# Performance work log

Hardware: AMD Instinct MI355X
Metric: run time of the kernel (lower is better)

Reference implementation:

```python
import jax, jax.numpy as jnp
import numpy as np

D_MODEL, D_INNER, D_STATE, HEADDIM, NHEADS, D_CONV, EPS = 2048, 4096, 64, 64, 64, 4, 1e-5
CONV_DIM = D_INNER + 2 * D_STATE  # ngroups=1


def setup_inputs() -> dict:
    key = jax.random.key(0)
    ks = jax.random.split(key, 8)
    return {
        "hidden_states": jax.random.normal(ks[0], (2, 2048, D_MODEL), jnp.float32),
        "rms_weight": jnp.ones((D_MODEL,), jnp.float32),
        "in_proj_w": jax.random.normal(ks[1], (2 * D_INNER + 2 * D_STATE + NHEADS, D_MODEL), jnp.float32) * 0.02,
        "conv_w": jax.random.normal(ks[2], (CONV_DIM, D_CONV), jnp.float32) * 0.2,
        "conv_b": jnp.zeros((CONV_DIM,), jnp.float32),
        "dt_bias": jax.random.normal(ks[3], (NHEADS,), jnp.float32) * 0.5,
        "A_log": jax.random.uniform(ks[4], (NHEADS,), jnp.float32, 0.0, 1.0),
        "D": jnp.ones((NHEADS,), jnp.float32),
        "norm_w": jnp.ones((D_INNER,), jnp.float32),
        "out_proj_w": jax.random.normal(ks[5], (D_MODEL, D_INNER), jnp.float32) * 0.02,
    }


def _rmsnorm(x, w, eps=EPS):
    var = jnp.mean(jnp.square(x), axis=-1, keepdims=True)
    return x * jax.lax.rsqrt(var + eps) * w


def reference(hidden_states, rms_weight, in_proj_w, conv_w, conv_b, dt_bias, A_log, D, norm_w, out_proj_w):
    b, l, _ = hidden_states.shape
    residual = hidden_states
    u = _rmsnorm(hidden_states, rms_weight)
    zxbcdt = jnp.einsum("bld,ed->ble", u, in_proj_w)
    z = zxbcdt[..., :D_INNER]
    xBC = zxbcdt[..., D_INNER:D_INNER + CONV_DIM]
    dt = zxbcdt[..., D_INNER + CONV_DIM:]  # (b, l, h)

    # causal depthwise conv1d over seq
    xBC_t = jnp.transpose(xBC, (0, 2, 1))  # (b, c, l)
    kernel = conv_w[:, None, :]  # (c, 1, k)
    xBC_t = jax.lax.conv_general_dilated(
        xBC_t, kernel, window_strides=(1,), padding=[(D_CONV - 1, 0)],
        feature_group_count=CONV_DIM,
        dimension_numbers=("NCH", "OIH", "NCH"))
    xBC = jax.nn.silu(jnp.transpose(xBC_t, (0, 2, 1)) + conv_b)

    x = xBC[..., :D_INNER].reshape(b, l, NHEADS, HEADDIM)
    B = xBC[..., D_INNER:D_INNER + D_STATE]  # (b, l, n)
    C = xBC[..., D_INNER + D_STATE:]         # (b, l, n)

    dt = jax.nn.softplus(dt + dt_bias)  # (b, l, h)
    A = -jnp.exp(A_log)                 # (h,)
    dA = jnp.exp(dt * A)                # (b, l, h)

    # sequential selective scan over time
    def step(state, inp):
        dA_t, dt_t, x_t, B_t, C_t = inp  # (b,h), (b,h), (b,h,p), (b,n), (b,n)
        state = state * dA_t[:, :, None, None] + jnp.einsum(
            "bh,bhp,bn->bhpn", dt_t, x_t, B_t)
        y_t = jnp.einsum("bhpn,bn->bhp", state, C_t)
        return state, y_t

    xs = (jnp.moveaxis(dA, 1, 0), jnp.moveaxis(dt, 1, 0),
          jnp.moveaxis(x, 1, 0), jnp.moveaxis(B, 1, 0), jnp.moveaxis(C, 1, 0))
    state0 = jnp.zeros((b, NHEADS, HEADDIM, D_STATE), hidden_states.dtype)
    _, ys = jax.lax.scan(step, state0, xs)
    y = jnp.moveaxis(ys, 0, 1)  # (b, l, h, p)
    y = y + D[None, None, :, None] * x
    y = y.reshape(b, l, D_INNER)

    # gated RMSNorm, then output projection
    y = _rmsnorm(y * jax.nn.silu(z), norm_w)
    out = jnp.einsum("ble,de->bld", y, out_proj_w)
    return residual + out
```

## Files before the change

kernel.cpp:

```cpp
#include <hip/hip_runtime.h>
#include <stdint.h>

#define DEV static __device__ __forceinline__

typedef __attribute__((ext_vector_type(8))) __bf16 bf16x8;
typedef __attribute__((ext_vector_type(4))) float f32x4;
typedef __attribute__((ext_vector_type(16))) float f32x16;

DEV float b2f(unsigned short u) {
    union { unsigned int i; float f; } v; v.i = ((unsigned int)u) << 16; return v.f;
}
DEV unsigned short f2b(float f) {
    unsigned int u = __builtin_bit_cast(unsigned int, f);
    unsigned int r = (u + 0x7FFFu + ((u >> 16) & 1u)) >> 16;
    return (unsigned short)r;
}
DEV f32x4 mfma16(bf16x8 a, bf16x8 b, f32x4 c) {
    return __builtin_amdgcn_mfma_f32_16x16x32_bf16(a, b, c, 0, 0, 0);
}
DEV f32x16 mfma32(bf16x8 a, bf16x8 b, f32x16 c) {
    return __builtin_amdgcn_mfma_f32_32x32x16_bf16(a, b, c, 0, 0, 0);
}

DEV void gload16(const void* g, void* l) {
    __builtin_amdgcn_global_load_lds(
        (const __attribute__((address_space(1))) void*)g,
        (__attribute__((address_space(3))) void*)l, 16, 0, 0);
}

__global__ __launch_bounds__(256) void k_cvt(
    const float* __restrict__ src, unsigned short* __restrict__ dst)
{
    long i = ((long)blockIdx.x * 256 + threadIdx.x) * 8;
    float4 a = *(const float4*)(src + i);
    float4 b = *(const float4*)(src + i + 4);
    union { uint4 v; unsigned short s[8]; } o;
    o.s[0] = f2b(a.x); o.s[1] = f2b(a.y); o.s[2] = f2b(a.z); o.s[3] = f2b(a.w);
    o.s[4] = f2b(b.x); o.s[5] = f2b(b.y); o.s[6] = f2b(b.z); o.s[7] = f2b(b.w);
    *(uint4*)(dst + i) = o.v;
}

__global__ __launch_bounds__(256) void k_rmsnorm_in(
    const float* __restrict__ h, const float* __restrict__ w,
    unsigned short* __restrict__ u)
{
    int row = blockIdx.x, t = threadIdx.x;
    const float* hp = h + (long)row * 2048 + t * 8;
    float4 a = *(const float4*)hp;
    float4 b = *(const float4*)(hp + 4);
    float x[8] = {a.x, a.y, a.z, a.w, b.x, b.y, b.z, b.w};
    float ss = 0.f;
#pragma unroll
    for (int i = 0; i < 8; i++) ss += x[i] * x[i];
#pragma unroll
    for (int o = 32; o > 0; o >>= 1) ss += __shfl_down(ss, o);
    __shared__ float red[4];
    if ((t & 63) == 0) red[t >> 6] = ss;
    __syncthreads();
    float tot = red[0] + red[1] + red[2] + red[3];
    float scale = rsqrtf(tot * (1.0f / 2048.0f) + 1e-5f);
    float4 wa = *(const float4*)(w + t * 8);
    float4 wb = *(const float4*)(w + t * 8 + 4);
    float wv[8] = {wa.x, wa.y, wa.z, wa.w, wb.x, wb.y, wb.z, wb.w};
    union { uint4 v; unsigned short s[8]; } ow;
#pragma unroll
    for (int i = 0; i < 8; i++) ow.s[i] = f2b(x[i] * scale * wv[i]);
    *(uint4*)(u + (long)row * 2048 + t * 8) = ow.v;
}

template <int EPI>
__global__ __launch_bounds__(256) void k_gemm_bt(
    const unsigned short* __restrict__ A, const unsigned short* __restrict__ Bm,
    int K, int nvalid, unsigned short* __restrict__ Cb, float* __restrict__ Cf,
    int ldc, const float* __restrict__ Res)
{
    __shared__ __align__(16) unsigned short sA[128 * 32];
    __shared__ __align__(16) unsigned short sB[128 * 32];
    int t = threadIdx.x;
    int w = t >> 6, L = t & 63;

    int flat = blockIdx.y * gridDim.x + blockIdx.x;
    int per = gridDim.x * 8;
    int strip = flat / per;
    int rem = flat - strip * per;
    long m0 = (long)(strip * 8 + (rem & 7)) * 128;
    long n0 = (long)(rem >> 3) * 128;

    int rS = w * 32 + (L >> 2);
    int cS = (L & 3) * 8;
    long rB0 = n0 + rS;       if (rB0 >= nvalid) rB0 = nvalid - 1;
    long rB1 = n0 + rS + 16;  if (rB1 >= nvalid) rB1 = nvalid - 1;
    const unsigned short* gA0 = A + (m0 + rS) * K + cS;
    const unsigned short* gA1 = gA0 + 16L * K;
    const unsigned short* gB0 = Bm + rB0 * K + cS;
    const unsigned short* gB1 = Bm + rB1 * K + cS;
    unsigned short* lA0 = sA + (w * 32) * 32 + L * 8;
    unsigned short* lA1 = lA0 + 16 * 32;
    unsigned short* lB0 = sB + (w * 32) * 32 + L * 8;
    unsigned short* lB1 = lB0 + 16 * 32;

    int mw = (w >> 1) * 64, nw = (w & 1) * 64;
    const unsigned short* fA = sA + (mw + (L & 31)) * 32 + (L >> 5) * 8;
    const unsigned short* fB = sB + (nw + (L & 31)) * 32 + (L >> 5) * 8;

    f32x16 acc[2][2];
#pragma unroll
    for (int ti = 0; ti < 2; ti++)
#pragma unroll
        for (int tj = 0; tj < 2; tj++)
#pragma unroll
            for (int r = 0; r < 16; r++) acc[ti][tj][r] = 0.f;

    for (int kt = 0; kt < K; kt += 32) {
        gload16(gA0, lA0); gload16(gA1, lA1);
        gload16(gB0, lB0); gload16(gB1, lB1);
        gA0 += 32; gA1 += 32; gB0 += 32; gB1 += 32;
        __syncthreads();
#pragma unroll
        for (int kk = 0; kk < 2; kk++) {
            bf16x8 af[2], bf[2];
#pragma unroll
            for (int ti = 0; ti < 2; ti++)
                af[ti] = *(const bf16x8*)(fA + ti * 32 * 32 + kk * 16);
#pragma unroll
            for (int tj = 0; tj < 2; tj++)
                bf[tj] = *(const bf16x8*)(fB + tj * 32 * 32 + kk * 16);
#pragma unroll
            for (int ti = 0; ti < 2; ti++)
#pragma unroll
                for (int tj = 0; tj < 2; tj++)
                    acc[ti][tj] = mfma32(af[ti], bf[tj], acc[ti][tj]);
        }
        __syncthreads();
    }
    int colL = L & 31;
    int rL = (L >> 5) * 4;
#pragma unroll
    for (int ti = 0; ti < 2; ti++)
#pragma unroll
        for (int tj = 0; tj < 2; tj++) {
            long c = n0 + nw + tj * 32 + colL;
            if (c >= nvalid) continue;
#pragma unroll
            for (int r = 0; r < 16; r++) {
                long row = m0 + mw + ti * 32 + (r & 3) + 8 * (r >> 2) + rL;
                float v = acc[ti][tj][r];
                if (EPI == 0) Cb[row * ldc + c] = f2b(v);
                else          Cf[row * ldc + c] = v + Res[row * ldc + c];
            }
        }
}

__global__ __launch_bounds__(128) void k_conv(
    const unsigned short* __restrict__ zx, const float* __restrict__ cw,
    const float* __restrict__ cb, unsigned short* __restrict__ xbc)
{
    int c = blockIdx.x * 128 + threadIdx.x;
    int b = blockIdx.z;
    int l0 = blockIdx.y * 64;
    float w0 = cw[c * 4 + 0], w1 = cw[c * 4 + 1];
    float w2 = cw[c * 4 + 2], w3 = cw[c * 4 + 3];
    float bias = cb[c];
    const unsigned short* src = zx + ((long)b * 2048) * 8384 + 4096 + c;
    float xm3 = (l0 >= 3) ? b2f(src[(long)(l0 - 3) * 8384]) : 0.f;
    float xm2 = (l0 >= 2) ? b2f(src[(long)(l0 - 2) * 8384]) : 0.f;
    float xm1 = (l0 >= 1) ? b2f(src[(long)(l0 - 1) * 8384]) : 0.f;
    const unsigned short* s2 = src + (long)l0 * 8384;
    unsigned short* dst = xbc + ((long)(b * 2048 + l0)) * 4224 + c;
#pragma unroll 8
    for (int i = 0; i < 64; i++) {
        float xl = b2f(*s2); s2 += 8384;
        float a = xm3 * w0 + xm2 * w1 + xm1 * w2 + xl * w3 + bias;
        a = a / (1.f + expf(-a));
        *dst = f2b(a); dst += 4224;
        xm3 = xm2; xm2 = xm1; xm1 = xl;
    }
}

__global__ __launch_bounds__(256) void k_chunk_state_mfma(
    const unsigned short* __restrict__ xbc, const unsigned short* __restrict__ zxdt,
    const float* __restrict__ dt_bias, const float* __restrict__ A_log,
    unsigned short* __restrict__ Sbuf, float* __restrict__ dAtot)
{
    int blk = blockIdx.x;
    int c = blk & 7, bh = blk >> 3;
    int b = bh >> 6, h = bh & 63;
    int tid = threadIdx.x;
    int w = tid >> 6, L = tid & 63;
    int quad = L >> 4, col = L & 15;
    int rowBlk = (w >> 1) * 32, colBlk = (w & 1) * 32;
    __shared__ __align__(16) unsigned short sXp[64 * 72];
    __shared__ __align__(16) unsigned short sBn[64 * 72];
    __shared__ float sdt[64], sL[64];
    float Ah = expf(A_log[h]);
    float dtb = dt_bias[h];
    f32x4 acc[2][2];
#pragma unroll
    for (int ti = 0; ti < 2; ti++)
#pragma unroll
        for (int tj = 0; tj < 2; tj++) acc[ti][tj] = (f32x4){0.f, 0.f, 0.f, 0.f};
    float sumL = 0.f;

    for (int sub = 0; sub < 4; sub++) {
        int l0 = c * 256 + sub * 64;
        {
            int t = tid >> 2, pc = tid & 3;
            const unsigned short* gX = xbc + (long)(b * 2048 + l0 + t) * 4224 + h * 64 + pc * 16;
            union { uint4 v; unsigned short s[8]; } x0, x1;
            x0.v = *(const uint4*)gX; x1.v = *(const uint4*)(gX + 8);
#pragma unroll
            for (int j = 0; j < 8; j++) {
                sXp[(pc * 16 + j) * 72 + t] = x0.s[j];
                sXp[(pc * 16 + 8 + j) * 72 + t] = x1.s[j];
            }
        }
        if (tid < 64) {
            float raw = b2f(zxdt[((long)(b * 2048 + l0 + tid)) * 8384 + 8320 + h]) + dtb;
            float dtv = (raw > 20.f) ? raw : log1pf(expf(raw));
            float cum = dtv;
#pragma unroll
            for (int off = 1; off < 64; off <<= 1) {
                float v = __shfl_up(cum, off);
                if (tid >= off) cum += v;
            }
            sdt[tid] = dtv;
            sL[tid] = -Ah * cum;
        }
        __syncthreads();
        float Lend = sL[63];
        {
            int t = tid >> 2, nc = tid & 3;
            float wt = sdt[t] * __expf(Lend - sL[t]);
            const unsigned short* gB = xbc + (long)(b * 2048 + l0 + t) * 4224 + 4096 + nc * 16;
            union { uint4 v; unsigned short s[8]; } x0, x1;
            x0.v = *(const uint4*)gB; x1.v = *(const uint4*)(gB + 8);
#pragma unroll
            for (int j = 0; j < 8; j++) {
                sBn[(nc * 16 + j) * 72 + t] = f2b(b2f(x0.s[j]) * wt);
                sBn[(nc * 16 + 8 + j) * 72 + t] = f2b(b2f(x1.s[j]) * wt);
            }
        }
        __syncthreads();
        float e_end = __expf(Lend);
        sumL += Lend;
#pragma unroll
        for (int ti = 0; ti < 2; ti++)
#pragma unroll
            for (int tj = 0; tj < 2; tj++)
#pragma unroll
                for (int r = 0; r < 4; r++) acc[ti][tj][r] *= e_end;
#pragma unroll
        for (int kb = 0; kb < 2; kb++) {
            bf16x8 ax[2], bx[2];
#pragma unroll
            for (int ti = 0; ti < 2; ti++)
                ax[ti] = *(const bf16x8*)(sXp + (rowBlk + ti * 16 + col) * 72 + kb * 32 + quad * 8);
#pragma unroll
            for (int tj = 0; tj < 2; tj++)
                bx[tj] = *(const bf16x8*)(sBn + (colBlk + tj * 16 + col) * 72 + kb * 32 + quad * 8);
#pragma unroll
            for (int ti = 0; ti < 2; ti++)
#pragma unroll
                for (int tj = 0; tj < 2; tj++)
                    acc[ti][tj] = mfma16(ax[ti], bx[tj], acc[ti][tj]);
        }
        __syncthreads();
    }
#pragma unroll
    for (int ti = 0; ti < 2; ti++)
#pragma unroll
        for (int tj = 0; tj < 2; tj++)
#pragma unroll
            for (int r = 0; r < 4; r++) {
                int p = rowBlk + ti * 16 + quad * 4 + r;
                int n = colBlk + tj * 16 + col;
                Sbuf[(long)blk * 4096 + p * 64 + n] = f2b(acc[ti][tj][r]);
            }
    if (tid == 0) dAtot[blk] = __expf(sumL);
}

__global__ __launch_bounds__(256) void k_scan_chunk_mfma(
    const unsigned short* __restrict__ xbc, const unsigned short* __restrict__ zxdt,
    const float* __restrict__ dt_bias, const float* __restrict__ A_log,
    const float* __restrict__ Dv,
    const unsigned short* __restrict__ Sbuf, const float* __restrict__ dAtot,
    unsigned short* __restrict__ yout)
{
    int blk = blockIdx.x;
    int c = blk & 7, bh = blk >> 3;
    int b = bh >> 6, h = bh & 63;
    int tid = threadIdx.x;
    int w = tid >> 6, L = tid & 63;
    int quad = L >> 4, col = L & 15;
    int rowBlk = (w >> 1) * 32, colBlk = (w & 1) * 32;
    __shared__ __align__(16) unsigned short sCm[64 * 72];
    __shared__ __align__(16) unsigned short sBtMs[64 * 72];
    __shared__ __align__(16) unsigned short sXp[64 * 72];
    __shared__ __align__(16) unsigned short sBn[64 * 72];
    __shared__ __align__(16) unsigned short sHb[64 * 72];
    __shared__ float sdt[64], sL[64], sEs[64];
    float Ah = expf(A_log[h]);
    float dtb = dt_bias[h];
    float Dh = Dv[h];

    f32x4 acc_h[2][2];
#pragma unroll
    for (int ti = 0; ti < 2; ti++)
#pragma unroll
        for (int tj = 0; tj < 2; tj++) acc_h[ti][tj] = (f32x4){0.f, 0.f, 0.f, 0.f};
    int sb = bh * 8;
    for (int j = 0; j < c; j++) {
        float d = dAtot[sb + j];
        const unsigned short* Sp = Sbuf + (long)(sb + j) * 4096;
#pragma unroll
        for (int ti = 0; ti < 2; ti++)
#pragma unroll
            for (int tj = 0; tj < 2; tj++)
#pragma unroll
                for (int r = 0; r < 4; r++) {
                    int p = rowBlk + ti * 16 + quad * 4 + r;
                    int n = colBlk + tj * 16 + col;
                    acc_h[ti][tj][r] = acc_h[ti][tj][r] * d + b2f(Sp[p * 64 + n]);
                }
    }

    for (int sub = 0; sub < 4; sub++) {
        int l0 = c * 256 + sub * 64;
        {
            int row = tid >> 2, c4 = tid & 3;
            const unsigned short* gR = xbc + (long)(b * 2048 + l0 + row) * 4224;
            uint4 v0 = *(const uint4*)(gR + 4160 + c4 * 8);
            uint4 v1 = *(const uint4*)(gR + 4160 + (c4 + 4) * 8);
            *(uint4*)(sCm + row * 72 + c4 * 8) = v0;
            *(uint4*)(sCm + row * 72 + (c4 + 4) * 8) = v1;
            uint4 w0 = *(const uint4*)(gR + 4096 + c4 * 8);
            uint4 w1 = *(const uint4*)(gR + 4096 + (c4 + 4) * 8);
            *(uint4*)(sBtMs + row * 72 + c4 * 8) = w0;
            *(uint4*)(sBtMs + row * 72 + (c4 + 4) * 8) = w1;
        }
        {
            int t = tid >> 2, pc = tid & 3;
            const unsigned short* gX = xbc + (long)(b * 2048 + l0 + t) * 4224 + h * 64 + pc * 16;
            union { uint4 v; unsigned short s[8]; } x0, x1;
            x0.v = *(const uint4*)gX; x1.v = *(const uint4*)(gX + 8);
#pragma unroll
            for (int j = 0; j < 8; j++) {
                sXp[(pc * 16 + j) * 72 + t] = x0.s[j];
                sXp[(pc * 16 + 8 + j) * 72 + t] = x1.s[j];
            }
        }
        if (tid < 64) {
            float raw = b2f(zxdt[((long)(b * 2048 + l0 + tid)) * 8384 + 8320 + h]) + dtb;
            float dtv = (raw > 20.f) ? raw : log1pf(expf(raw));
            float cum = dtv;
#pragma unroll
            for (int off = 1; off < 64; off <<= 1) {
                float v = __shfl_up(cum, off);
                if (tid >= off) cum += v;
            }
            sdt[tid] = dtv;
            float l = -Ah * cum;
            sL[tid] = l;
            sEs[tid] = __expf(l);
        }
        __syncthreads();
        float Lend = sL[63];
        {
            int t = tid >> 2, nc = tid & 3;
            float wt = sdt[t] * __expf(Lend - sL[t]);
            const unsigned short* gB = xbc + (long)(b * 2048 + l0 + t) * 4224 + 4096 + nc * 16;
            union { uint4 v; unsigned short s[8]; } x0, x1;
            x0.v = *(const uint4*)gB; x1.v = *(const uint4*)(gB + 8);
#pragma unroll
            for (int j = 0; j < 8; j++) {
                sBn[(nc * 16 + j) * 72 + t] = f2b(b2f(x0.s[j]) * wt);
                sBn[(nc * 16 + 8 + j) * 72 + t] = f2b(b2f(x1.s[j]) * wt);
            }
        }
#pragma unroll
        for (int ti = 0; ti < 2; ti++)
#pragma unroll
            for (int tj = 0; tj < 2; tj++)
#pragma unroll
                for (int r = 0; r < 4; r++) {
                    int p = rowBlk + ti * 16 + quad * 4 + r;
                    int n = colBlk + tj * 16 + col;
                    sHb[p * 72 + n] = f2b(acc_h[ti][tj][r]);
                }
        __syncthreads();
        f32x4 g[2][2];
#pragma unroll
        for (int ti = 0; ti < 2; ti++)
#pragma unroll
            for (int tj = 0; tj < 2; tj++) g[ti][tj] = (f32x4){0.f, 0.f, 0.f, 0.f};
#pragma unroll
        for (int kb = 0; kb < 2; kb++) {
            bf16x8 ac[2], bc[2];
#pragma unroll
            for (int ti = 0; ti < 2; ti++)
                ac[ti] = *(const bf16x8*)(sCm + (rowBlk + ti * 16 + col) * 72 + kb * 32 + quad * 8);
#pragma unroll
            for (int tj = 0; tj < 2; tj++)
                bc[tj] = *(const bf16x8*)(sBtMs + (colBlk + tj * 16 + col) * 72 + kb * 32 + quad * 8);
#pragma unroll
            for (int ti = 0; ti < 2; ti++)
#pragma unroll
                for (int tj = 0; tj < 2; tj++)
                    g[ti][tj] = mfma16(ac[ti], bc[tj], g[ti][tj]);
        }
        __syncthreads();
#pragma unroll
        for (int tj = 0; tj < 2; tj++) {
            int t_idx = colBlk + tj * 16 + col;
            float lt = sL[t_idx], dtt = sdt[t_idx];
#pragma unroll
            for (int ti = 0; ti < 2; ti++)
#pragma unroll
                for (int r = 0; r < 4; r++) {
                    int s_idx = rowBlk + ti * 16 + quad * 4 + r;
                    float m = (t_idx <= s_idx) ? g[ti][tj][r] * dtt * __expf(sL[s_idx] - lt) : 0.f;
                    sBtMs[s_idx * 72 + t_idx] = f2b(m);
                }
        }
        __syncthreads();
        f32x4 yv[2][2];
#pragma unroll
        for (int ti = 0; ti < 2; ti++)
#pragma unroll
            for (int tj = 0; tj < 2; tj++) yv[ti][tj] = (f32x4){0.f, 0.f, 0.f, 0.f};
#pragma unroll
        for (int kb = 0; kb < 2; kb++) {
            bf16x8 am[2], bxp[2];
#pragma unroll
            for (int ti = 0; ti < 2; ti++)
                am[ti] = *(const bf16x8*)(sBtMs + (rowBlk + ti * 16 + col) * 72 + kb * 32 + quad * 8);
#pragma unroll
            for (int tj = 0; tj < 2; tj++)
                bxp[tj] = *(const bf16x8*)(sXp + (colBlk + tj * 16 + col) * 72 + kb * 32 + quad * 8);
#pragma unroll
            for (int ti = 0; ti < 2; ti++)
#pragma unroll
                for (int tj = 0; tj < 2; tj++)
                    yv[ti][tj] = mfma16(am[ti], bxp[tj], yv[ti][tj]);
        }
        float es0 = sEs[rowBlk + col], es1 = sEs[rowBlk + 16 + col];
#pragma unroll
        for (int kb = 0; kb < 2; kb++) {
            bf16x8 acx[2], bhh[2];
#pragma unroll
            for (int ti = 0; ti < 2; ti++) {
                union { bf16x8 v; unsigned short s[8]; } a;
                a.v = *(const bf16x8*)(sCm + (rowBlk + ti * 16 + col) * 72 + kb * 32 + quad * 8);
                float es = ti ? es1 : es0;
#pragma unroll
                for (int j = 0; j < 8; j++) a.s[j] = f2b(b2f(a.s[j]) * es);
                acx[ti] = a.v;
            }
#pragma unroll
            for (int tj = 0; tj < 2; tj++)
                bhh[tj] = *(const bf16x8*)(sHb + (colBlk + tj * 16 + col) * 72 + kb * 32 + quad * 8);
#pragma unroll
            for (int ti = 0; ti < 2; ti++)
#pragma unroll
                for (int tj = 0; tj < 2; tj++)
                    yv[ti][tj] = mfma16(acx[ti], bhh[tj], yv[ti][tj]);
        }
        float e_end = __expf(Lend);
#pragma unroll
        for (int ti = 0; ti < 2; ti++)
#pragma unroll
            for (int tj = 0; tj < 2; tj++)
#pragma unroll
                for (int r = 0; r < 4; r++) acc_h[ti][tj][r] *= e_end;
#pragma unroll
        for (int kb = 0; kb < 2; kb++) {
            bf16x8 ax[2], bn[2];
#pragma unroll
            for (int ti = 0; ti < 2; ti++)
                ax[ti] = *(const bf16x8*)(sXp + (rowBlk + ti * 16 + col) * 72 + kb * 32 + quad * 8);
#pragma unroll
            for (int tj = 0; tj < 2; tj++)
                bn[tj] = *(const bf16x8*)(sBn + (colBlk + tj * 16 + col) * 72 + kb * 32 + quad * 8);
#pragma unroll
            for (int ti = 0; ti < 2; ti++)
#pragma unroll
                for (int tj = 0; tj < 2; tj++)
                    acc_h[ti][tj] = mfma16(ax[ti], bn[tj], acc_h[ti][tj]);
        }
#pragma unroll
        for (int ti = 0; ti < 2; ti++)
#pragma unroll
            for (int tj = 0; tj < 2; tj++)
#pragma unroll
                for (int r = 0; r < 4; r++) {
                    int s_idx = rowBlk + ti * 16 + quad * 4 + r;
                    int p = colBlk + tj * 16 + col;
                    float xv = b2f(sXp[p * 72 + s_idx]);
                    float yo = yv[ti][tj][r] + Dh * xv;
                    yout[((long)(b * 2048 + l0 + s_idx)) * 8384 + 4096 + h * 64 + p] = f2b(yo);
                }
        __syncthreads();
    }
}

__global__ __launch_bounds__(256) void k_gatenorm(
    const unsigned short* __restrict__ zx, const float* __restrict__ nw,
    unsigned short* __restrict__ y2)
{
    int row = blockIdx.x, t = threadIdx.x;
    const unsigned short* zr = zx + (long)row * 8384;
    float v[16]; float ss = 0.f;
#pragma unroll
    for (int i = 0; i < 16; i++) {
        int c = t + i * 256;
        float z = b2f(zr[c]);
        float y = b2f(zr[4096 + c]);
        float g = y * (z / (1.f + expf(-z)));
        v[i] = g; ss += g * g;
    }
#pragma unroll
    for (int o = 32; o > 0; o >>= 1) ss += __shfl_down(ss, o);
    __shared__ float red[4];
    if ((t & 63) == 0) red[t >> 6] = ss;
    __syncthreads();
    float tot = red[0] + red[1] + red[2] + red[3];
    float scale = rsqrtf(tot * (1.0f / 4096.0f) + 1e-5f);
#pragma unroll
    for (int i = 0; i < 16; i++) {
        int c = t + i * 256;
        y2[(long)row * 4096 + c] = f2b(v[i] * scale * nw[c]);
    }
}

extern "C" void kernel_launch(void* const* d_in, const int* in_sizes, int n_in,
                              void* d_out, int out_size, void* d_ws, size_t ws_size,
                              hipStream_t stream)
{
    const float* h    = (const float*)d_in[0];
    const float* rmsw = (const float*)d_in[1];
    const float* w1   = (const float*)d_in[2];
    const float* cw   = (const float*)d_in[3];
    const float* cbp  = (const float*)d_in[4];
    const float* dtb  = (const float*)d_in[5];
    const float* alog = (const float*)d_in[6];
    const float* Dv   = (const float*)d_in[7];
    const float* nw   = (const float*)d_in[8];
    const float* w2   = (const float*)d_in[9];

    char* ws = (char*)d_ws;
    unsigned short* zx    = (unsigned short*)ws;
    unsigned short* w1b   = (unsigned short*)(ws + 68681728L);
    unsigned short* xbc   = (unsigned short*)(ws + 68681728L);
    unsigned short* y2    = (unsigned short*)(ws + 68681728L);
    unsigned short* u     = (unsigned short*)(ws + 103284736L);
    unsigned short* Sbuf  = (unsigned short*)(ws + 103284736L);
    float*          dAt   = (float*)(ws + 111673344L);
    unsigned short* w2b   = (unsigned short*)(ws + 103284736L);
    float* outp = (float*)d_out;

    k_rmsnorm_in<<<4096, 256, 0, stream>>>(h, rmsw, u);
    k_cvt<<<8384, 256, 0, stream>>>(w1, w1b);
    k_gemm_bt<0><<<dim3(66, 32), 256, 0, stream>>>(u, w1b, 2048, 8384, zx, nullptr, 8384, nullptr);
    k_conv<<<dim3(33, 32, 2), 128, 0, stream>>>(zx, cw, cbp, xbc);
    k_chunk_state_mfma<<<1024, 256, 0, stream>>>(xbc, zx, dtb, alog, Sbuf, dAt);
    k_scan_chunk_mfma<<<1024, 256, 0, stream>>>(xbc, zx, dtb, alog, Dv, Sbuf, dAt, zx);
    k_gatenorm<<<4096, 256, 0, stream>>>(zx, nw, y2);
    k_cvt<<<4096, 256, 0, stream>>>(w2, w2b);
    k_gemm_bt<1><<<dim3(16, 32), 256, 0, stream>>>(y2, w2b, 4096, 2048, nullptr, outp, 2048, h);
}
```

Before: 583.3 us.

## Double GEMM K-tile to 64 and XOR-swizzle shared memory layout

Measured after the change: 552.6 us. -5.3%, faster.

```diff
diff --git a/kernel.cpp b/kernel.cpp
--- a/kernel.cpp
+++ b/kernel.cpp
@@ -74,8 +74,8 @@
     int K, int nvalid, unsigned short* __restrict__ Cb, float* __restrict__ Cf,
     int ldc, const float* __restrict__ Res)
 {
-    __shared__ __align__(16) unsigned short sA[128 * 32];
-    __shared__ __align__(16) unsigned short sB[128 * 32];
+    __shared__ __align__(16) unsigned short sA[128 * 64];
+    __shared__ __align__(16) unsigned short sB[128 * 64];
     int t = threadIdx.x;
     int w = t >> 6, L = t & 63;
 
@@ -86,22 +86,27 @@
     long m0 = (long)(strip * 8 + (rem & 7)) * 128;
     long n0 = (long)(rem >> 3) * 128;
 
-    int rS = w * 32 + (L >> 2);
-    int cS = (L & 3) * 8;
-    long rB0 = n0 + rS;       if (rB0 >= nvalid) rB0 = nvalid - 1;
-    long rB1 = n0 + rS + 16;  if (rB1 >= nvalid) rB1 = nvalid - 1;
-    const unsigned short* gA0 = A + (m0 + rS) * K + cS;
-    const unsigned short* gA1 = gA0 + 16L * K;
-    const unsigned short* gB0 = Bm + rB0 * K + cS;
-    const unsigned short* gB1 = Bm + rB1 * K + cS;
-    unsigned short* lA0 = sA + (w * 32) * 32 + L * 8;
-    unsigned short* lA1 = lA0 + 16 * 32;
-    unsigned short* lB0 = sB + (w * 32) * 32 + L * 8;
-    unsigned short* lB1 = lB0 + 16 * 32;
+    int rloc = t >> 3;
+    int c16  = t & 7;
+    int csw  = c16 ^ (rloc & 7);
+    const unsigned short* gAp[4];
+    const unsigned short* gBp[4];
+#pragma unroll
+    for (int i = 0; i < 4; i++) {
+        gAp[i] = A + (m0 + i * 32 + rloc) * (long)K + csw * 8;
+        long rb = n0 + i * 32 + rloc;
+        if (rb >= nvalid) rb = nvalid - 1;
+        gBp[i] = Bm + rb * (long)K + csw * 8;
+    }
+    unsigned short* lA = sA + t * 8;
+    unsigned short* lB = sB + t * 8;
 
     int mw = (w >> 1) * 64, nw = (w & 1) * 64;
-    const unsigned short* fA = sA + (mw + (L & 31)) * 32 + (L >> 5) * 8;
-    const unsigned short* fB = sB + (nw + (L & 31)) * 32 + (L >> 5) * 8;
+    int rowA = mw + (L & 31), rowB = nw + (L & 31);
+    int swA = (rowA & 7) << 4, swB = (rowB & 7) << 4;
+    int q16 = (L >> 5) * 16;
+    const char* pA = (const char*)sA + rowA * 128;
+    const char* pB = (const char*)sB + rowB * 128;
 
     f32x16 acc[2][2];
 #pragma unroll
@@ -111,20 +116,23 @@
 #pragma unroll
             for (int r = 0; r < 16; r++) acc[ti][tj][r] = 0.f;
 
-    for (int kt = 0; kt < K; kt += 32) {
-        gload16(gA0, lA0); gload16(gA1, lA1);
-        gload16(gB0, lB0); gload16(gB1, lB1);
-        gA0 += 32; gA1 += 32; gB0 += 32; gB1 += 32;
-        __syncthreads();
-#pragma unroll
-        for (int kk = 0; kk < 2; kk++) {
+    for (int kt = 0; kt < K; kt += 64) {
+#pragma unroll
+        for (int i = 0; i < 4; i++) {
+            gload16(gAp[i], lA + i * 2048);
+            gload16(gBp[i], lB + i * 2048);
+            gAp[i] += 64; gBp[i] += 64;
+        }
+        __syncthreads();
+#pragma unroll
+        for (int kk = 0; kk < 4; kk++) {
             bf16x8 af[2], bf[2];
 #pragma unroll
             for (int ti = 0; ti < 2; ti++)
-                af[ti] = *(const bf16x8*)(fA + ti * 32 * 32 + kk * 16);
-#pragma unroll
-            for (int tj = 0; tj < 2; tj++)
-                bf[tj] = *(const bf16x8*)(fB + tj * 32 * 32 + kk * 16);
+                af[ti] = *(const bf16x8*)(pA + ti * 4096 + ((q16 + kk * 32) ^ swA));
+#pragma unroll
+            for (int tj = 0; tj < 2; tj++)
+                bf[tj] = *(const bf16x8*)(pB + tj * 4096 + ((q16 + kk * 32) ^ swB));
 #pragma unroll
             for (int ti = 0; ti < 2; ti++)
 #pragma unroll
```
